# Kernel optimization log

Measured on AMD Instinct MI355X. Metric: run time of the kernel, lower is better.

## Reference

```python
import jax, jax.numpy as jnp
import numpy as np

N = 50000      # nodes
E = 800000     # edges
IN = 32        # raw node feature dim
PE = 15        # laplacian PE dim (k)
HID = 128      # hidden
HEADS = 4
C = HID // HEADS
G = 64         # graphs in batch
L = 4          # num layers (shared weights!)


def setup_inputs() -> dict:
    key = jax.random.key(0)
    ks = jax.random.split(key, 24)
    s = 0.05
    p = lambda k, shape: jax.random.normal(k, shape, dtype=jnp.float32) * s
    inp = {
        "x": jax.random.normal(ks[0], (N, IN), dtype=jnp.float32),
        "edge_index": jax.random.randint(ks[1], (2, E), 0, N, dtype=jnp.int32),
        "batch": jnp.sort(jax.random.randint(ks[2], (N,), 0, G, dtype=jnp.int32)),
        "lap_pe": jax.random.normal(ks[3], (N, PE), dtype=jnp.float32),
        # node_in: Linear(IN+PE -> HID)
        "node_in_w": p(ks[4], (HID, IN + PE)), "node_in_b": p(ks[5], (HID,)),
        # shared TransformerConv params
        "Wq": p(ks[6], (HID, HID)), "bq": p(ks[7], (HID,)),
        "Wk": p(ks[8], (HID, HID)), "bk": p(ks[9], (HID,)),
        "Wv": p(ks[10], (HID, HID)), "bv": p(ks[11], (HID,)),
        "Wskip": p(ks[12], (HID, HID)), "bskip": p(ks[13], (HID,)),
        "Wbeta": p(ks[14], (1, 3 * HID)),  # bias=False in PyG
        # attentional aggregation gate: Linear(HID,HID)->ReLU->Linear(HID,1)
        "g1_w": p(ks[15], (HID, HID)), "g1_b": p(ks[16], (HID,)),
        "g2_w": p(ks[17], (1, HID)), "g2_b": p(ks[18], (1,)),
        # readout: Linear(HID,HID)->ReLU->Linear(HID,1)
        "r1_w": p(ks[19], (HID, HID)), "r1_b": p(ks[20], (HID,)),
        "r2_w": p(ks[21], (1, HID)), "r2_b": p(ks[22], (1,)),
    }
    return inp


def _transformer_conv(x, src, dst, Wq, bq, Wk, bk, Wv, bv, Wskip, bskip, Wbeta):
    # projections -> [N, HEADS, C]
    q = (x @ Wq.T + bq).reshape(N, HEADS, C)
    k = (x @ Wk.T + bk).reshape(N, HEADS, C)
    v = (x @ Wv.T + bv).reshape(N, HEADS, C)
    # edge attention logits: [E, HEADS]
    alpha = jnp.einsum('ehc,ehc->eh', q[dst], k[src]) / jnp.sqrt(jnp.float32(C))
    # segment softmax over destination node
    amax = jax.ops.segment_max(alpha, dst, num_segments=N)        # [N, HEADS]
    ex = jnp.exp(alpha - amax[dst])
    denom = jax.ops.segment_sum(ex, dst, num_segments=N)          # [N, HEADS]
    attn = ex / denom[dst]                                        # [E, HEADS]
    # weighted scatter-add of values
    msg = v[src] * attn[:, :, None]                               # [E, HEADS, C]
    out = jax.ops.segment_sum(msg, dst, num_segments=N).reshape(N, HID)
    # beta-gated skip connection (beta=True, root_weight=True)
    x_r = x @ Wskip.T + bskip
    beta = jax.nn.sigmoid(jnp.concatenate([out, x_r, out - x_r], axis=-1) @ Wbeta.T)
    return beta * x_r + (1.0 - beta) * out


def reference(x, edge_index, batch, lap_pe, node_in_w, node_in_b,
              Wq, bq, Wk, bk, Wv, bv, Wskip, bskip, Wbeta,
              g1_w, g1_b, g2_w, g2_b, r1_w, r1_b, r2_w, r2_b):
    src, dst = edge_index[0], edge_index[1]
    h = jnp.concatenate([x, lap_pe], axis=-1) @ node_in_w.T + node_in_b  # [N, HID]
    for _ in range(L):  # same conv instance reused -> shared weights
        h = jax.nn.relu(h + _transformer_conv(h, src, dst, Wq, bq, Wk, bk,
                                              Wv, bv, Wskip, bskip, Wbeta))
    # attentional aggregation over graphs
    gate = jax.nn.relu(h @ g1_w.T + g1_b) @ g2_w.T + g2_b                # [N, 1]
    gmax = jax.ops.segment_max(gate, batch, num_segments=G)
    gex = jnp.exp(gate - gmax[batch])
    gden = jax.ops.segment_sum(gex, batch, num_segments=G)
    w = gex / gden[batch]                                                # [N, 1]
    g = jax.ops.segment_sum(w * h, batch, num_segments=G)                # [G, HID]
    out = jax.nn.relu(g @ r1_w.T + r1_b) @ r2_w.T + r2_b                 # [G, 1]
    return out.squeeze(-1)
```

## Files before the change

kernel.cpp:

```cpp
#include <hip/hip_runtime.h>

#define NN 50000
#define EE 800000
#define INF 32
#define PEF 15
#define HID 128
#define GG 64
#define NLAYERS 4
#define NBLK 196

typedef __bf16 bf16;
typedef __attribute__((ext_vector_type(8))) bf16 bf16x8;
typedef __attribute__((ext_vector_type(4))) float f32x4;
typedef __attribute__((ext_vector_type(2))) float f32x2;

__device__ __forceinline__ float wave_allsum(float v) {
  #pragma unroll
  for (int off = 1; off < 64; off <<= 1) v += __shfl_xor(v, off);
  return v;
}

__device__ __forceinline__ float bflo(unsigned u) {
  return __builtin_bit_cast(float, u << 16);
}
__device__ __forceinline__ float bfhi(unsigned u) {
  return __builtin_bit_cast(float, u & 0xffff0000u);
}
__device__ __forceinline__ unsigned short f2bf(float v) {
  unsigned b = __builtin_bit_cast(unsigned, v);
  unsigned r = (b + 0x7fffu + ((b >> 16) & 1u)) >> 16;
  return (unsigned short)r;
}
__device__ __forceinline__ unsigned bfpack(float lo, float hi) {
  return (unsigned)f2bf(lo) | ((unsigned)f2bf(hi) << 16);
}
__device__ __forceinline__ unsigned fp8pack4(float a, float b, float c, float d) {
  unsigned lo = (unsigned)__builtin_amdgcn_cvt_pk_fp8_f32(a, b, 0, false) & 0xffffu;
  unsigned hi = (unsigned)__builtin_amdgcn_cvt_pk_fp8_f32(c, d, 0, false) & 0xffffu;
  return lo | (hi << 16);
}

__global__ void pack_weights_kernel(const float* __restrict__ Wq, const float* __restrict__ Wk,
                                    const float* __restrict__ Wv, const float* __restrict__ Ws,
                                    const float* __restrict__ bq, const float* __restrict__ bk,
                                    const float* __restrict__ bv, const float* __restrict__ bs,
                                    unsigned short* __restrict__ Wcatb, float* __restrict__ bcat) {
  int idx = blockIdx.x * blockDim.x + threadIdx.x;
  if (idx >= 512 * 128) return;
  int o = idx >> 7, j = idx & 127;
  int w = o >> 7, r = o & 127;
  const float* W = (w == 0) ? Wq : (w == 1) ? Wk : (w == 2) ? Wv : Ws;
  Wcatb[idx] = f2bf(W[r * 128 + j]);
  if (j == 0) {
    const float* b = (w == 0) ? bq : (w == 1) ? bk : (w == 2) ? bv : bs;
    bcat[o] = b[r];
  }
}

__global__ void pack_nwtb_kernel(const float* __restrict__ niw, unsigned short* __restrict__ nwtb) {
  int idx = blockIdx.x * blockDim.x + threadIdx.x;
  if (idx >= 128 * 64) return;
  int n = idx >> 6, j = idx & 63;
  nwtb[idx] = (j < INF + PEF) ? f2bf(niw[n * (INF + PEF) + j]) : (unsigned short)0;
}

__global__ void pack_g1_kernel(const float* __restrict__ g1w, unsigned short* __restrict__ g1wb) {
  int idx = blockIdx.x * blockDim.x + threadIdx.x;
  if (idx >= 128 * 128) return;
  g1wb[idx] = f2bf(g1w[idx]);
}

__global__ __launch_bounds__(256) void xpe_pack_kernel(const float* __restrict__ x,
    const float* __restrict__ pe, unsigned* __restrict__ xpeb4) {
  int n = blockIdx.x * 256 + threadIdx.x;
  if (n >= NN) return;
  unsigned ou[32];
  const float4* xr = (const float4*)(x + (size_t)n * INF);
  #pragma unroll
  for (int i = 0; i < 8; i++) {
    float4 v = xr[i];
    ou[2 * i] = bfpack(v.x, v.y);
    ou[2 * i + 1] = bfpack(v.z, v.w);
  }
  const float* pr = pe + (size_t)n * PEF;
  float p[16];
  #pragma unroll
  for (int i = 0; i < PEF; i++) p[i] = pr[i];
  p[15] = 0.f;
  #pragma unroll
  for (int i = 0; i < 8; i++) ou[16 + i] = bfpack(p[2 * i], p[2 * i + 1]);
  #pragma unroll
  for (int i = 24; i < 32; i++) ou[i] = 0u;
  unsigned* dst = xpeb4 + (size_t)n * 32;
  #pragma unroll
  for (int i = 0; i < 8; i++) ((uint4*)dst)[i] = *(uint4*)&ou[4 * i];
}

__global__ __launch_bounds__(256) void nodein_gemm_kernel(
    const bf16* __restrict__ A, const bf16* __restrict__ B,
    const float* __restrict__ bias, int M,
    float* __restrict__ h, unsigned* __restrict__ hbf4) {
  __shared__ float lds[128 * 64];
  const int t = threadIdx.x;
  const int w = t >> 6, lane = t & 63;
  const int m0 = blockIdx.x * 128;
  const int n0 = blockIdx.y * 64;
  const int lrow = lane & 15, lk = (lane >> 4) * 8;
  int ra = m0 + w * 32 + lrow;      if (ra > M - 1) ra = M - 1;
  int rb = m0 + w * 32 + 16 + lrow; if (rb > M - 1) rb = M - 1;
  const bf16* a0p = A + (size_t)ra * 64 + lk;
  const bf16* a1p = A + (size_t)rb * 64 + lk;
  const bf16* bp  = B + (size_t)(n0 + lrow) * 64 + lk;
  f32x4 acc[2][4] = {};
  #pragma unroll
  for (int ks = 0; ks < 2; ks++) {
    bf16x8 a0 = *(const bf16x8*)(a0p + ks * 32);
    bf16x8 a1 = *(const bf16x8*)(a1p + ks * 32);
    #pragma unroll
    for (int nj = 0; nj < 4; nj++) {
      bf16x8 b = *(const bf16x8*)(bp + (size_t)nj * 1024 + ks * 32);
      acc[0][nj] = __builtin_amdgcn_mfma_f32_16x16x32_bf16(a0, b, acc[0][nj], 0, 0, 0);
      acc[1][nj] = __builtin_amdgcn_mfma_f32_16x16x32_bf16(a1, b, acc[1][nj], 0, 0, 0);
    }
  }
  const int rbase = (lane >> 4) * 4;
  #pragma unroll
  for (int mi = 0; mi < 2; mi++) {
    #pragma unroll
    for (int nj = 0; nj < 4; nj++) {
      #pragma unroll
      for (int r = 0; r < 4; r++) {
        int ml = w * 32 + mi * 16 + rbase + r;
        int col = nj * 16 + lrow;
        lds[ml * 64 + (col ^ ((ml & 7) << 2))] = acc[mi][nj][r] + bias[n0 + col];
      }
    }
  }
  __syncthreads();
  #pragma unroll
  for (int kk = 0; kk < 2; kk++) {
    int u = t + kk * 256;
    int r = u & 127, s = u >> 7;
    int m = m0 + r;
    if (m >= M) continue;
    float ff[16];
    #pragma unroll
    for (int j = 0; j < 4; j++) {
      int c = s * 16 + j * 4;
      *(float4*)(ff + j * 4) = *(const float4*)(lds + r * 64 + (c ^ ((r & 7) << 2)));
    }
    int c0 = n0 + s * 16;
    float4* hp = (float4*)(h + (size_t)m * 128 + c0);
    #pragma unroll
    for (int j = 0; j < 4; j++) hp[j] = *(float4*)(ff + j * 4);
    unsigned o[8];
    #pragma unroll
    for (int i = 0; i < 8; i++) o[i] = bfpack(ff[2 * i], ff[2 * i + 1]);
    uint4* hb = (uint4*)(hbf4 + (size_t)m * 64 + (c0 >> 1));
    hb[0] = *(uint4*)&o[0];
    hb[1] = *(uint4*)&o[4];
  }
}

__global__ void count_kernel(const int* __restrict__ dst, int* __restrict__ counts) {
  int e = blockIdx.x * blockDim.x + threadIdx.x;
  if (e >= EE) return;
  atomicAdd(&counts[dst[e]], 1);
}

__global__ __launch_bounds__(256) void bsum_kernel(const int* __restrict__ counts,
                                                   int* __restrict__ bsum) {
  int b = blockIdx.x, t = threadIdx.x;
  int i = b * 256 + t;
  int v = (i < NN) ? counts[i] : 0;
  #pragma unroll
  for (int off = 1; off < 64; off <<= 1) v += __shfl_xor(v, off);
  __shared__ int red[4];
  if ((t & 63) == 0) red[t >> 6] = v;
  __syncthreads();
  if (t == 0) bsum[b] = red[0] + red[1] + red[2] + red[3];
}

__global__ void bscan_kernel(const int* __restrict__ bsum, int* __restrict__ bbase) {
  int lane = threadIdx.x;
  int carry = 0;
  for (int c = 0; c < NBLK; c += 64) {
    int i = c + lane;
    int v = (i < NBLK) ? bsum[i] : 0;
    int x = v;
    #pragma unroll
    for (int off = 1; off < 64; off <<= 1) {
      int u = __shfl_up(x, off);
      if (lane >= off) x += u;
    }
    if (i < NBLK) bbase[i] = carry + x - v;
    carry += __shfl(x, 63);
  }
}

__global__ __launch_bounds__(256) void rowptr_kernel(const int* __restrict__ counts,
    const int* __restrict__ bbase, int* __restrict__ row_ptr, int* __restrict__ cursor) {
  int b = blockIdx.x, t = threadIdx.x;
  int lane = t & 63, wid = t >> 6;
  int i = b * 256 + t;
  int v = (i < NN) ? counts[i] : 0;
  int x = v;
  #pragma unroll
  for (int off = 1; off < 64; off <<= 1) {
    int u = __shfl_up(x, off);
    if (lane >= off) x += u;
  }
  __shared__ int wsum[4];
  if (lane == 63) wsum[wid] = x;
  __syncthreads();
  int offs = bbase[b];
  for (int k = 0; k < wid; k++) offs += wsum[k];
  int incl = offs + x;
  if (i < NN) { row_ptr[i + 1] = incl; cursor[i] = incl - v; }
  if (b == 0 && t == 0) row_ptr[0] = 0;
}

__global__ void scatter_kernel(const int* __restrict__ src, const int* __restrict__ dst,
                               int* __restrict__ cursor, int* __restrict__ srcs) {
  int e = blockIdx.x * blockDim.x + threadIdx.x;
  if (e >= EE) return;
  int d = dst[e];
  int p = atomicAdd(&cursor[d], 1);
  srcs[p] = src[e];
}

__global__ void gptr_kernel(const int* __restrict__ batch, int* __restrict__ gptr) {
  int g = threadIdx.x;
  if (g > GG) return;
  if (g == GG) { gptr[GG] = NN; return; }
  int lo = 0, hi = NN;
  while (lo < hi) {
    int mid = (lo + hi) >> 1;
    if (batch[mid] < g) lo = mid + 1; else hi = mid;
  }
  gptr[g] = lo;
}

__global__ __launch_bounds__(256) void gemm0_kernel(
    const bf16* __restrict__ A, const bf16* __restrict__ B,
    const float* __restrict__ bias, int M,
    unsigned short* __restrict__ qbb, unsigned char* __restrict__ kvb,
    unsigned short* __restrict__ xrbb) {
  __shared__ float lds[128 * 64];
  const int t = threadIdx.x;
  const int w = t >> 6, lane = t & 63;
  const int m0 = blockIdx.x * 128;
  const int by = blockIdx.y;
  const int n0 = by * 64;
  const int lrow = lane & 15, lk = (lane >> 4) * 8;
  int ra = m0 + w * 32 + lrow;      if (ra > M - 1) ra = M - 1;
  int rb = m0 + w * 32 + 16 + lrow; if (rb > M - 1) rb = M - 1;
  const bf16* a0p = A + (size_t)ra * 128 + lk;
  const bf16* a1p = A + (size_t)rb * 128 + lk;
  const bf16* bp  = B + (size_t)(n0 + lrow) * 128 + lk;
  f32x4 acc[2][4] = {};
  #pragma unroll
  for (int ks = 0; ks < 4; ks++) {
    bf16x8 a0 = *(const bf16x8*)(a0p + ks * 32);
    bf16x8 a1 = *(const bf16x8*)(a1p + ks * 32);
    #pragma unroll
    for (int nj = 0; nj < 4; nj++) {
      bf16x8 b = *(const bf16x8*)(bp + (size_t)nj * 2048 + ks * 32);
      acc[0][nj] = __builtin_amdgcn_mfma_f32_16x16x32_bf16(a0, b, acc[0][nj], 0, 0, 0);
      acc[1][nj] = __builtin_amdgcn_mfma_f32_16x16x32_bf16(a1, b, acc[1][nj], 0, 0, 0);
    }
  }
  const int rbase = (lane >> 4) * 4;
  #pragma unroll
  for (int mi = 0; mi < 2; mi++) {
    #pragma unroll
    for (int nj = 0; nj < 4; nj++) {
      #pragma unroll
      for (int r = 0; r < 4; r++) {
        int ml = w * 32 + mi * 16 + rbase + r;
        int col = nj * 16 + lrow;
        lds[ml * 64 + (col ^ ((ml & 7) << 2))] = acc[mi][nj][r] + bias[n0 + col];
      }
    }
  }
  __syncthreads();
  #pragma unroll
  for (int kk = 0; kk < 2; kk++) {
    int u = t + kk * 256;
    int r = u & 127, s = u >> 7;
    int m = m0 + r;
    float ff[16];
    #pragma unroll
    for (int j = 0; j < 4; j++) {
      int c = s * 16 + j * 4;
      *(float4*)(ff + j * 4) = *(const float4*)(lds + r * 64 + (c ^ ((r & 7) << 2)));
    }
    if (m < M) {
      int c0 = (by & 1) * 64 + s * 16;
      if (by < 2) {
        unsigned o[8];
        #pragma unroll
        for (int i = 0; i < 8; i++) o[i] = bfpack(ff[2 * i], ff[2 * i + 1]);
        uint4* dst = (uint4*)(qbb + (size_t)m * 128 + c0);
        dst[0] = *(uint4*)&o[0];
        dst[1] = *(uint4*)&o[4];
      } else if (by < 6) {
        unsigned o[4];
        #pragma unroll
        for (int i = 0; i < 4; i++)
          o[i] = fp8pack4(ff[4 * i], ff[4 * i + 1], ff[4 * i + 2], ff[4 * i + 3]);
        int cell = c0 >> 3;
        int voff = (by < 4) ? 0 : 8;
        unsigned char* bp8 = kvb + (size_t)m * 256;
        uint2 w0; w0.x = o[0]; w0.y = o[1];
        uint2 w1; w1.x = o[2]; w1.y = o[3];
        *(uint2*)(bp8 + cell * 16 + voff) = w0;
        *(uint2*)(bp8 + (cell + 1) * 16 + voff) = w1;
      } else {
        unsigned o[8];
        #pragma unroll
        for (int i = 0; i < 8; i++) o[i] = bfpack(ff[2 * i], ff[2 * i + 1]);
        uint4* dst = (uint4*)(xrbb + (size_t)m * 128 + c0);
        dst[0] = *(uint4*)&o[0];
        dst[1] = *(uint4*)&o[4];
      }
    }
  }
}

__global__ __launch_bounds__(512) void gemm1_gate_kernel(
    const bf16* __restrict__ A, const bf16* __restrict__ B,
    const float* __restrict__ b1, const float* __restrict__ g2w,
    const float* __restrict__ g2b, int M, float* __restrict__ gx) {
  const int w = threadIdx.x >> 6, lane = threadIdx.x & 63;
  const int m0 = blockIdx.x * 128 + w * 16;
  const int lrow = lane & 15, lk = (lane >> 4) * 8;
  int ra = m0 + lrow; if (ra > M - 1) ra = M - 1;
  const bf16* ap = A + (size_t)ra * 128 + lk;
  const bf16* bp = B + (size_t)lrow * 128 + lk;
  f32x4 acc[8] = {};
  #pragma unroll
  for (int ks = 0; ks < 4; ks++) {
    bf16x8 a = *(const bf16x8*)(ap + ks * 32);
    #pragma unroll
    for (int nj = 0; nj < 8; nj++) {
      bf16x8 b = *(const bf16x8*)(bp + (size_t)nj * 2048 + ks * 32);
      acc[nj] = __builtin_amdgcn_mfma_f32_16x16x32_bf16(a, b, acc[nj], 0, 0, 0);
    }
  }
  float g2v[8], b1v[8];
  #pragma unroll
  for (int nj = 0; nj < 8; nj++) {
    g2v[nj] = g2w[nj * 16 + lrow];
    b1v[nj] = b1[nj * 16 + lrow];
  }
  const float b2 = g2b[0];
  const int rbase = (lane >> 4) * 4;
  #pragma unroll
  for (int r = 0; r < 4; r++) {
    int m = m0 + rbase + r;
    float d = 0.f;
    #pragma unroll
    for (int nj = 0; nj < 8; nj++)
      d += fmaxf(acc[nj][r] + b1v[nj], 0.f) * g2v[nj];
    d += __shfl_xor(d, 1);
    d += __shfl_xor(d, 2);
    d += __shfl_xor(d, 4);
    d += __shfl_xor(d, 8);
    if (lrow == 0 && m < M) gx[m] = __expf(d + b2);
  }
}

__global__ __launch_bounds__(256) void attn_beta_kernel(
    const unsigned short* __restrict__ qbb,
    const unsigned char* __restrict__ kvb,
    const int* __restrict__ row_ptr, const int* __restrict__ srcs,
    const unsigned* __restrict__ xrb4,
    const float* __restrict__ Wbeta,
    float* __restrict__ h, unsigned* __restrict__ hbf4) {
  __shared__ float xlds[4][128];
  const int wid = threadIdx.x >> 6;
  const int wv = blockIdx.x * 4 + wid;
  const int lane = threadIdx.x & 63;
  const int sl = lane & 15;
  const int eg = lane >> 4;
  float qf[8];
  {
    bf16x8 qv = *(const bf16x8*)((const bf16*)qbb + (size_t)wv * 128 + sl * 8);
    #pragma unroll
    for (int j = 0; j < 8; j++) qf[j] = (float)qv[j];
  }
  const int e0 = row_ptr[wv], e1 = row_ptr[wv + 1];
  const float C = 0.25503486f;
  float dex = 0.f;
  float acc[8] = {0, 0, 0, 0, 0, 0, 0, 0};

#define PROC(cell, valid)                                                   \
  {                                                                         \
    f32x2 k0 = __builtin_amdgcn_cvt_pk_f32_fp8((cell).x, false);            \
    f32x2 k1 = __builtin_amdgcn_cvt_pk_f32_fp8((cell).x, true);             \
    f32x2 k2 = __builtin_amdgcn_cvt_pk_f32_fp8((cell).y, false);            \
    f32x2 k3 = __builtin_amdgcn_cvt_pk_f32_fp8((cell).y, true);             \
    float p = qf[0] * k0.x + qf[1] * k0.y + qf[2] * k1.x + qf[3] * k1.y     \
            + qf[4] * k2.x + qf[5] * k2.y + qf[6] * k3.x + qf[7] * k3.y;    \
    p += __shfl_xor(p, 1);                                                  \
    p += __shfl_xor(p, 2);                                                  \
    float ex = (valid) ? exp2f(p * C) : 0.f;                                \
    dex += ex;                                                              \
    f32x2 v0 = __builtin_amdgcn_cvt_pk_f32_fp8((cell).z, false);            \
    f32x2 v1 = __builtin_amdgcn_cvt_pk_f32_fp8((cell).z, true);             \
    f32x2 v2 = __builtin_amdgcn_cvt_pk_f32_fp8((cell).w, false);            \
    f32x2 v3 = __builtin_amdgcn_cvt_pk_f32_fp8((cell).w, true);             \
    acc[0] += ex * v0.x; acc[1] += ex * v0.y;                               \
    acc[2] += ex * v1.x; acc[3] += ex * v1.y;                               \
    acc[4] += ex * v2.x; acc[5] += ex * v2.y;                               \
    acc[6] += ex * v3.x; acc[7] += ex * v3.y;                               \
  }

  for (int base = e0; base < e1; base += 64) {
    int rem = e1 - base;
    int cnt = rem < 64 ? rem : 64;
    int mysrc = (lane < rem) ? srcs[base + lane] : 0;
    int i = 0;
    for (; i + 4 < cnt; i += 8) {
      int sea = __shfl(mysrc, i + eg);
      int seb = __shfl(mysrc, i + 4 + eg);
      uint4 ca = *(const uint4*)(kvb + (size_t)sea * 256 + sl * 16);
      uint4 cb = *(const uint4*)(kvb + (size_t)seb * 256 + sl * 16);
      PROC(ca, true);
      PROC(cb, (i + 4 + eg < cnt));
    }
    if (i < cnt) {
      int sea = __shfl(mysrc, i + eg);
      uint4 ca = *(const uint4*)(kvb + (size_t)sea * 256 + sl * 16);
      PROC(ca, (i + eg < cnt));
    }
  }
#undef PROC

  dex += __shfl_xor(dex, 16);
  dex += __shfl_xor(dex, 32);
  #pragma unroll
  for (int j = 0; j < 8; j++) {
    acc[j] += __shfl_xor(acc[j], 16);
    acc[j] += __shfl_xor(acc[j], 32);
  }
  float inv = (e1 > e0) ? 1.f / dex : 0.f;
  if (eg == 0) {
    #pragma unroll
    for (int j = 0; j < 8; j++) xlds[wid][sl * 8 + j] = acc[j] * inv;
  }
  __syncthreads();
  float ox = xlds[wid][2 * lane];
  float oy = xlds[wid][2 * lane + 1];
  unsigned xu = xrb4[(size_t)wv * 64 + lane];
  float xx = bflo(xu), xy = bfhi(xu);
  const float2* wb = (const float2*)Wbeta;
  float2 wo = wb[lane], wx = wb[64 + lane], wd = wb[128 + lane];
  float part = ox * wo.x + oy * wo.y + xx * wx.x + xy * wx.y
             + (ox - xx) * wd.x + (oy - xy) * wd.y;
  part = wave_allsum(part);
  float beta = 1.f / (1.f + __expf(-part));
  float2* hp = (float2*)(h + (size_t)wv * 128);
  float2 h2 = hp[lane];
  float r0 = fmaxf(h2.x + beta * xx + (1.f - beta) * ox, 0.f);
  float r1 = fmaxf(h2.y + beta * xy + (1.f - beta) * oy, 0.f);
  h2.x = r0; h2.y = r1;
  hp[lane] = h2;
  hbf4[(size_t)wv * 64 + lane] = bfpack(r0, r1);
}

__global__ __launch_bounds__(256) void gden_kernel(const float* __restrict__ gx,
    const int* __restrict__ gptr, float* __restrict__ gden) {
  int g = blockIdx.x, t = threadIdx.x;
  int n0 = gptr[g], n1 = gptr[g + 1];
  float s = 0.f;
  for (int n = n0 + t; n < n1; n += 256) s += gx[n];
  s = wave_allsum(s);
  __shared__ float red[4];
  if ((t & 63) == 0) red[t >> 6] = s;
  __syncthreads();
  if (t == 0) gden[g] = red[0] + red[1] + red[2] + red[3];
}

__global__ __launch_bounds__(128) void gagg_kernel(const float* __restrict__ gx,
    const float* __restrict__ h, const int* __restrict__ gptr,
    float* __restrict__ gfeat_raw) {
  int g = blockIdx.x;
  int c = blockIdx.y;
  int d = threadIdx.x;
  int n0 = gptr[g], n1 = gptr[g + 1];
  float acc = 0.f;
  for (int n = n0 + c; n < n1; n += 32) acc += gx[n] * h[(size_t)n * 128 + d];
  atomicAdd(&gfeat_raw[g * 128 + d], acc);
}

__global__ __launch_bounds__(128) void readout_kernel(const float* __restrict__ gfeat_raw,
    const float* __restrict__ gden,
    const float* __restrict__ r1w, const float* __restrict__ r1b,
    const float* __restrict__ r2w, const float* __restrict__ r2b,
    float* __restrict__ out) {
  int g = blockIdx.x;
  int u = threadIdx.x;
  __shared__ float sh[128];
  __shared__ float red[128];
  float dv = gden[g];
  float inv = (dv > 0.f) ? 1.f / dv : 0.f;
  sh[u] = gfeat_raw[g * 128 + u] * inv;
  __syncthreads();
  float tacc = r1b[u];
  for (int j = 0; j < 128; j++) tacc += sh[j] * r1w[u * 128 + j];
  tacc = fmaxf(tacc, 0.f);
  red[u] = tacc * r2w[u];
  __syncthreads();
  for (int off = 64; off > 0; off >>= 1) {
    if (u < off) red[u] += red[u + off];
    __syncthreads();
  }
  if (u == 0) out[g] = red[0] + r2b[0];
}

extern "C" void kernel_launch(void* const* d_in, const int* in_sizes, int n_in,
                              void* d_out, int out_size, void* d_ws, size_t ws_size,
                              hipStream_t stream) {
  (void)in_sizes; (void)n_in; (void)out_size; (void)ws_size;
  const float* x     = (const float*)d_in[0];
  const int*   ei    = (const int*)d_in[1];
  const int*   batch = (const int*)d_in[2];
  const float* pe    = (const float*)d_in[3];
  const float* niw   = (const float*)d_in[4];
  const float* nib   = (const float*)d_in[5];
  const float* Wq    = (const float*)d_in[6];
  const float* bq    = (const float*)d_in[7];
  const float* Wk    = (const float*)d_in[8];
  const float* bk    = (const float*)d_in[9];
  const float* Wv    = (const float*)d_in[10];
  const float* bv    = (const float*)d_in[11];
  const float* Wsk   = (const float*)d_in[12];
  const float* bsk   = (const float*)d_in[13];
  const float* Wbeta = (const float*)d_in[14];
  const float* g1w   = (const float*)d_in[15];
  const float* g1b   = (const float*)d_in[16];
  const float* g2w   = (const float*)d_in[17];
  const float* g2b   = (const float*)d_in[18];
  const float* r1w   = (const float*)d_in[19];
  const float* r1b   = (const float*)d_in[20];
  const float* r2w   = (const float*)d_in[21];
  const float* r2b   = (const float*)d_in[22];
  float* out = (float*)d_out;

  float* ws = (float*)d_ws;
  float* h     = ws; ws += (size_t)NN * 128;
  float* qbbf  = ws; ws += (size_t)NN * 64;
  float* kvbf  = ws; ws += (size_t)NN * 64;
  float* xrbf  = ws; ws += (size_t)NN * 64;
  float* hbff  = ws; ws += (size_t)NN * 64;
  float* xpebf = ws; ws += (size_t)NN * 32;
  float* Wcatf = ws; ws += 512 * 64;
  float* g1wbf = ws; ws += 128 * 64;
  float* nwtbf = ws; ws += 128 * 32;
  float* bcat  = ws; ws += 512;
  float* gx    = ws; ws += NN;
  float* gfeat = ws; ws += GG * 128;
  float* gden  = ws; ws += GG;
  int* row_ptr = (int*)ws;
  int* counts  = row_ptr + (NN + 1);
  int* cursor  = counts + NN;
  int* srcs    = cursor + NN;
  int* gptr    = srcs + EE;
  int* bsum    = gptr + (GG + 1);
  int* bbase   = bsum + 256;

  unsigned short* qbb   = (unsigned short*)qbbf;
  unsigned char*  kvb   = (unsigned char*)kvbf;
  unsigned short* xrbb  = (unsigned short*)xrbf;
  unsigned short* hbf   = (unsigned short*)hbff;
  unsigned short* Wcatb = (unsigned short*)Wcatf;
  unsigned short* g1wb  = (unsigned short*)g1wbf;
  unsigned short* nwtb  = (unsigned short*)nwtbf;
  const int* src = ei;
  const int* dst = ei + EE;

  hipMemsetAsync(counts, 0, NN * sizeof(int), stream);
  hipMemsetAsync(gfeat, 0, GG * 128 * sizeof(float), stream);
  pack_weights_kernel<<<(512 * 128 + 255) / 256, 256, 0, stream>>>(
      Wq, Wk, Wv, Wsk, bq, bk, bv, bsk, Wcatb, bcat);
  pack_nwtb_kernel<<<(128 * 64 + 255) / 256, 256, 0, stream>>>(niw, nwtb);
  pack_g1_kernel<<<(128 * 128 + 255) / 256, 256, 0, stream>>>(g1w, g1wb);
  xpe_pack_kernel<<<NBLK, 256, 0, stream>>>(x, pe, (unsigned*)xpebf);
  count_kernel<<<(EE + 255) / 256, 256, 0, stream>>>(dst, counts);
  bsum_kernel<<<NBLK, 256, 0, stream>>>(counts, bsum);
  bscan_kernel<<<1, 64, 0, stream>>>(bsum, bbase);
  rowptr_kernel<<<NBLK, 256, 0, stream>>>(counts, bbase, row_ptr, cursor);
  scatter_kernel<<<(EE + 255) / 256, 256, 0, stream>>>(src, dst, cursor, srcs);
  gptr_kernel<<<1, 128, 0, stream>>>(batch, gptr);

  const int MB0 = (NN + 127) / 128;
  nodein_gemm_kernel<<<dim3(MB0, 2), 256, 0, stream>>>(
      (const bf16*)xpebf, (const bf16*)nwtb, nib, NN, h, (unsigned*)hbf);

  for (int l = 0; l < NLAYERS; l++) {
    gemm0_kernel<<<dim3(MB0, 8), 256, 0, stream>>>(
        (const bf16*)hbf, (const bf16*)Wcatb, bcat, NN, qbb, kvb, xrbb);
    attn_beta_kernel<<<12500, 256, 0, stream>>>(
        qbb, kvb, row_ptr, srcs, (const unsigned*)xrbb, Wbeta, h, (unsigned*)hbf);
  }

  gemm1_gate_kernel<<<MB0, 512, 0, stream>>>(
      (const bf16*)hbf, (const bf16*)g1wb, g1b, g2w, g2b, NN, gx);
  gden_kernel<<<GG, 256, 0, stream>>>(gx, gptr, gden);
  gagg_kernel<<<dim3(GG, 32), 128, 0, stream>>>(gx, h, gptr, gfeat);
  readout_kernel<<<GG, 128, 0, stream>>>(gfeat, gden, r1w, r1b, r2w, r2b, out);
}
```

Baseline: 552.7 us.

## Bucketed two-pass CSR build with 16-bit sources and full-width gemm0 tiles

Replaces the per-edge global atomic scatter with a two-pass bucketed counting sort. Edges are first binned into 1024-node buckets with block-local LDS atomics, then placed into CSR order using LDS cursors per bucket, and source indices are stored as 16-bit values to shrink gather index traffic. gemm0 now runs one 512-thread block per 64 rows that computes all 512 output columns, instead of an 8-way grid over column tiles, so the A tile is read once per block. Adds more launches and LDS round trips with extra barriers. Storing sources in 16 bits assumes node ids fit in that width, but NN=50000 fits.

```diff
diff --git a/kernel.cpp b/kernel.cpp
--- a/kernel.cpp
+++ b/kernel.cpp
@@ -8,6 +8,9 @@
 #define GG 64
 #define NLAYERS 4
 #define NBLK 196
+#define NBUCK 49
+#define ECH 4096
+#define EBLK 196
 
 typedef __bf16 bf16;
 typedef __attribute__((ext_vector_type(8))) bf16 bf16x8;
@@ -199,7 +202,7 @@
 }
 
 __global__ __launch_bounds__(256) void rowptr_kernel(const int* __restrict__ counts,
-    const int* __restrict__ bbase, int* __restrict__ row_ptr, int* __restrict__ cursor) {
+    const int* __restrict__ bbase, int* __restrict__ row_ptr) {
   int b = blockIdx.x, t = threadIdx.x;
   int lane = t & 63, wid = t >> 6;
   int i = b * 256 + t;
@@ -216,17 +219,80 @@
   int offs = bbase[b];
   for (int k = 0; k < wid; k++) offs += wsum[k];
   int incl = offs + x;
-  if (i < NN) { row_ptr[i + 1] = incl; cursor[i] = incl - v; }
+  if (i < NN) row_ptr[i + 1] = incl;
   if (b == 0 && t == 0) row_ptr[0] = 0;
 }
 
-__global__ void scatter_kernel(const int* __restrict__ src, const int* __restrict__ dst,
-                               int* __restrict__ cursor, int* __restrict__ srcs) {
-  int e = blockIdx.x * blockDim.x + threadIdx.x;
-  if (e >= EE) return;
-  int d = dst[e];
-  int p = atomicAdd(&cursor[d], 1);
-  srcs[p] = src[e];
+__global__ __launch_bounds__(256) void binhist_kernel(const int* __restrict__ dst,
+                                                      int* __restrict__ blockHist) {
+  __shared__ int hist[NBUCK];
+  int t = threadIdx.x;
+  if (t < NBUCK) hist[t] = 0;
+  __syncthreads();
+  int base = blockIdx.x * ECH;
+  int end = base + ECH; if (end > EE) end = EE;
+  for (int i = base + t; i < end; i += 256) atomicAdd(&hist[dst[i] >> 10], 1);
+  __syncthreads();
+  if (t < NBUCK) blockHist[blockIdx.x * NBUCK + t] = hist[t];
+}
+
+__global__ void bscan2_kernel(const int* __restrict__ blockHist,
+    int* __restrict__ blockBase, int* __restrict__ bucket_base) {
+  int t = threadIdx.x;
+  int tot = 0;
+  if (t < NBUCK)
+    for (int b = 0; b < EBLK; b++) tot += blockHist[b * NBUCK + t];
+  int x = tot;
+  #pragma unroll
+  for (int off = 1; off < 64; off <<= 1) {
+    int u = __shfl_up(x, off);
+    if (t >= off) x += u;
+  }
+  int excl = x - tot;
+  if (t < NBUCK) bucket_base[t] = excl;
+  if (t == NBUCK - 1) bucket_base[NBUCK] = excl + tot;
+  if (t < NBUCK) {
+    int run = excl;
+    for (int b = 0; b < EBLK; b++) {
+      blockBase[b * NBUCK + t] = run;
+      run += blockHist[b * NBUCK + t];
+    }
+  }
+}
+
+__global__ __launch_bounds__(256) void binwrite_kernel(const int* __restrict__ src,
+    const int* __restrict__ dst, const int* __restrict__ blockBase,
+    unsigned* __restrict__ binned) {
+  __shared__ int cur[NBUCK];
+  int t = threadIdx.x;
+  if (t < NBUCK) cur[t] = blockBase[blockIdx.x * NBUCK + t];
+  __syncthreads();
+  int base = blockIdx.x * ECH;
+  int end = base + ECH; if (end > EE) end = EE;
+  for (int i = base + t; i < end; i += 256) {
+    int d = dst[i];
+    int p = atomicAdd(&cur[d >> 10], 1);
+    binned[p] = (unsigned)src[i] | ((unsigned)(d & 1023) << 16);
+  }
+}
+
+__global__ __launch_bounds__(512) void scatter2_kernel(const unsigned* __restrict__ binned,
+    const int* __restrict__ row_ptr, const int* __restrict__ bucket_base,
+    unsigned short* __restrict__ srcs16) {
+  __shared__ int cur[1024];
+  int g = blockIdx.x, t = threadIdx.x;
+  int nbase = g << 10;
+  for (int j = t; j < 1024; j += 512) {
+    int node = nbase + j;
+    cur[j] = (node < NN) ? row_ptr[node] : 0;
+  }
+  __syncthreads();
+  int s0 = bucket_base[g], s1 = bucket_base[g + 1];
+  for (int i = s0 + t; i < s1; i += 512) {
+    unsigned pr = binned[i];
+    int p = atomicAdd(&cur[pr >> 16], 1);
+    srcs16[p] = (unsigned short)(pr & 0xffffu);
+  }
 }
 
 __global__ void gptr_kernel(const int* __restrict__ batch, int* __restrict__ gptr) {
@@ -241,76 +307,78 @@
   gptr[g] = lo;
 }
 
-__global__ __launch_bounds__(256) void gemm0_kernel(
+__global__ __launch_bounds__(512) void gemm0_kernel(
     const bf16* __restrict__ A, const bf16* __restrict__ B,
     const float* __restrict__ bias, int M,
     unsigned short* __restrict__ qbb, unsigned char* __restrict__ kvb,
     unsigned short* __restrict__ xrbb) {
-  __shared__ float lds[128 * 64];
+  __shared__ float lds[64 * 128];
   const int t = threadIdx.x;
   const int w = t >> 6, lane = t & 63;
-  const int m0 = blockIdx.x * 128;
-  const int by = blockIdx.y;
-  const int n0 = by * 64;
+  const int wm = w >> 2, wn = w & 3;
+  const int mb = blockIdx.x * 64;
+  const int m0 = mb + wm * 32;
+  const int n0 = wn * 128;
   const int lrow = lane & 15, lk = (lane >> 4) * 8;
-  int ra = m0 + w * 32 + lrow;      if (ra > M - 1) ra = M - 1;
-  int rb = m0 + w * 32 + 16 + lrow; if (rb > M - 1) rb = M - 1;
+  int ra = m0 + lrow;      if (ra > M - 1) ra = M - 1;
+  int rb = m0 + 16 + lrow; if (rb > M - 1) rb = M - 1;
   const bf16* a0p = A + (size_t)ra * 128 + lk;
   const bf16* a1p = A + (size_t)rb * 128 + lk;
   const bf16* bp  = B + (size_t)(n0 + lrow) * 128 + lk;
-  f32x4 acc[2][4] = {};
+  f32x4 acc[2][8] = {};
   #pragma unroll
   for (int ks = 0; ks < 4; ks++) {
     bf16x8 a0 = *(const bf16x8*)(a0p + ks * 32);
     bf16x8 a1 = *(const bf16x8*)(a1p + ks * 32);
     #pragma unroll
-    for (int nj = 0; nj < 4; nj++) {
+    for (int nj = 0; nj < 8; nj++) {
       bf16x8 b = *(const bf16x8*)(bp + (size_t)nj * 2048 + ks * 32);
       acc[0][nj] = __builtin_amdgcn_mfma_f32_16x16x32_bf16(a0, b, acc[0][nj], 0, 0, 0);
       acc[1][nj] = __builtin_amdgcn_mfma_f32_16x16x32_bf16(a1, b, acc[1][nj], 0, 0, 0);
     }
   }
   const int rbase = (lane >> 4) * 4;
-  #pragma unroll
-  for (int mi = 0; mi < 2; mi++) {
-    #pragma unroll
-    for (int nj = 0; nj < 4; nj++) {
+  const int rr = t & 63, ss = t >> 6;
+  const int m = mb + rr;
+  #pragma unroll
+  for (int g = 0; g < 4; g++) {
+    if (wn == g) {
       #pragma unroll
-      for (int r = 0; r < 4; r++) {
-        int ml = w * 32 + mi * 16 + rbase + r;
-        int col = nj * 16 + lrow;
-        lds[ml * 64 + (col ^ ((ml & 7) << 2))] = acc[mi][nj][r] + bias[n0 + col];
+      for (int mi = 0; mi < 2; mi++) {
+        #pragma unroll
+        for (int nj = 0; nj < 8; nj++) {
+          #pragma unroll
+          for (int r = 0; r < 4; r++) {
+            int row = wm * 32 + mi * 16 + rbase + r;
+            int col = nj * 16 + lrow;
+            lds[row * 128 + (col ^ ((row & 7) << 2))] = acc[mi][nj][r] + bias[g * 128 + col];
+          }
+        }
       }
     }
-  }
-  __syncthreads();
-  #pragma unroll
-  for (int kk = 0; kk < 2; kk++) {
-    int u = t + kk * 256;
-    int r = u & 127, s = u >> 7;
-    int m = m0 + r;
-    float ff[16];
-    #pragma unroll
-    for (int j = 0; j < 4; j++) {
-      int c = s * 16 + j * 4;
-      *(float4*)(ff + j * 4) = *(const float4*)(lds + r * 64 + (c ^ ((r & 7) << 2)));
-    }
+    __syncthreads();
     if (m < M) {
-      int c0 = (by & 1) * 64 + s * 16;
-      if (by < 2) {
+      float ff[16];
+      #pragma unroll
+      for (int j = 0; j < 4; j++) {
+        int c = ss * 16 + j * 4;
+        *(float4*)(ff + j * 4) = *(const float4*)(lds + rr * 128 + (c ^ ((rr & 7) << 2)));
+      }
+      int c0 = ss * 16;
+      if (g == 0) {
         unsigned o[8];
         #pragma unroll
         for (int i = 0; i < 8; i++) o[i] = bfpack(ff[2 * i], ff[2 * i + 1]);
-        uint4* dst = (uint4*)(qbb + (size_t)m * 128 + c0);
-        dst[0] = *(uint4*)&o[0];
-        dst[1] = *(uint4*)&o[4];
-      } else if (by < 6) {
+        uint4* dq = (uint4*)(qbb + (size_t)m * 128 + c0);
+        dq[0] = *(uint4*)&o[0];
+        dq[1] = *(uint4*)&o[4];
+      } else if (g == 1 || g == 2) {
         unsigned o[4];
         #pragma unroll
         for (int i = 0; i < 4; i++)
           o[i] = fp8pack4(ff[4 * i], ff[4 * i + 1], ff[4 * i + 2], ff[4 * i + 3]);
         int cell = c0 >> 3;
-        int voff = (by < 4) ? 0 : 8;
+        int voff = (g == 1) ? 0 : 8;
         unsigned char* bp8 = kvb + (size_t)m * 256;
         uint2 w0; w0.x = o[0]; w0.y = o[1];
         uint2 w1; w1.x = o[2]; w1.y = o[3];
@@ -320,11 +388,12 @@
         unsigned o[8];
         #pragma unroll
         for (int i = 0; i < 8; i++) o[i] = bfpack(ff[2 * i], ff[2 * i + 1]);
-        uint4* dst = (uint4*)(xrbb + (size_t)m * 128 + c0);
-        dst[0] = *(uint4*)&o[0];
-        dst[1] = *(uint4*)&o[4];
+        uint4* dx = (uint4*)(xrbb + (size_t)m * 128 + c0);
+        dx[0] = *(uint4*)&o[0];
+        dx[1] = *(uint4*)&o[4];
       }
     }
+    __syncthreads();
   }
 }
 
@@ -374,7 +443,7 @@
 __global__ __launch_bounds__(256) void attn_beta_kernel(
     const unsigned short* __restrict__ qbb,
     const unsigned char* __restrict__ kvb,
-    const int* __restrict__ row_ptr, const int* __restrict__ srcs,
+    const int* __restrict__ row_ptr, const unsigned short* __restrict__ srcs,
     const unsigned* __restrict__ xrb4,
     const float* __restrict__ Wbeta,
     float* __restrict__ h, unsigned* __restrict__ hbf4) {
@@ -420,7 +489,7 @@
   for (int base = e0; base < e1; base += 64) {
     int rem = e1 - base;
     int cnt = rem < 64 ? rem : 64;
-    int mysrc = (lane < rem) ? srcs[base + lane] : 0;
+    int mysrc = (lane < rem) ? (int)srcs[base + lane] : 0;
     int i = 0;
     for (; i + 4 < cnt; i += 8) {
       int sea = __shfl(mysrc, i + eg);
@@ -564,12 +633,15 @@
   float* gfeat = ws; ws += GG * 128;
   float* gden  = ws; ws += GG;
   int* row_ptr = (int*)ws;
-  int* counts  = row_ptr + (NN + 1);
-  int* cursor  = counts + NN;
-  int* srcs    = cursor + NN;
-  int* gptr    = srcs + EE;
-  int* bsum    = gptr + (GG + 1);
-  int* bbase   = bsum + 256;
+  int* counts   = row_ptr + (NN + 1);
+  int* bsum     = counts + NN;
+  int* bbase    = bsum + NBLK;
+  int* gptr     = bbase + NBLK;
+  int* blockHist= gptr + (GG + 1);
+  int* blockBase= blockHist + EBLK * NBUCK;
+  int* bucketB  = blockBase + EBLK * NBUCK;
+  unsigned* binned = (unsigned*)(bucketB + (NBUCK + 1));
+  unsigned short* srcs16 = (unsigned short*)(binned + EE);
 
   unsigned short* qbb   = (unsigned short*)qbbf;
   unsigned char*  kvb   = (unsigned char*)kvbf;
@@ -591,19 +663,23 @@
   count_kernel<<<(EE + 255) / 256, 256, 0, stream>>>(dst, counts);
   bsum_kernel<<<NBLK, 256, 0, stream>>>(counts, bsum);
   bscan_kernel<<<1, 64, 0, stream>>>(bsum, bbase);
-  rowptr_kernel<<<NBLK, 256, 0, stream>>>(counts, bbase, row_ptr, cursor);
-  scatter_kernel<<<(EE + 255) / 256, 256, 0, stream>>>(src, dst, cursor, srcs);
+  rowptr_kernel<<<NBLK, 256, 0, stream>>>(counts, bbase, row_ptr);
+  binhist_kernel<<<EBLK, 256, 0, stream>>>(dst, blockHist);
+  bscan2_kernel<<<1, 64, 0, stream>>>(blockHist, blockBase, bucketB);
+  binwrite_kernel<<<EBLK, 256, 0, stream>>>(src, dst, blockBase, binned);
+  scatter2_kernel<<<NBUCK, 512, 0, stream>>>(binned, row_ptr, bucketB, srcs16);
   gptr_kernel<<<1, 128, 0, stream>>>(batch, gptr);
 
   const int MB0 = (NN + 127) / 128;
+  const int MB64 = (NN + 63) / 64;
   nodein_gemm_kernel<<<dim3(MB0, 2), 256, 0, stream>>>(
       (const bf16*)xpebf, (const bf16*)nwtb, nib, NN, h, (unsigned*)hbf);
 
   for (int l = 0; l < NLAYERS; l++) {
-    gemm0_kernel<<<dim3(MB0, 8), 256, 0, stream>>>(
+    gemm0_kernel<<<MB64, 512, 0, stream>>>(
         (const bf16*)hbf, (const bf16*)Wcatb, bcat, NN, qbb, kvb, xrbb);
     attn_beta_kernel<<<12500, 256, 0, stream>>>(
-        qbb, kvb, row_ptr, srcs, (const unsigned*)xrbb, Wbeta, h, (unsigned*)hbf);
+        qbb, kvb, row_ptr, srcs16, (const unsigned*)xrbb, Wbeta, h, (unsigned*)hbf);
   }
 
   gemm1_gate_kernel<<<MB0, 512, 0, stream>>>(
```

After: 623.6 us. +12.8%, slower.
